# Kernel optimization log

Measured on AMD Instinct MI355X. Metric: run time of the kernel, lower is better.

The kernel has to match this reference:

```python
import jax, jax.numpy as jnp
import numpy as np

# ---- MERU-style Lorentz geometry helpers (space components, implicit time) ----

def _time(x, curv):
    # x: [..., D] space component; time = sqrt(1/curv + ||x||^2)
    return jnp.sqrt(1.0 / curv + jnp.sum(x * x, axis=-1))


def pairwise_dist(x, y, curv, eps=1e-8):
    # Lorentzian inner product for all pairs: <x,y>_L = x.y - x_t*y_t  -> [N, M]
    xt = _time(x, curv)
    yt = _time(y, curv)
    inner = jnp.einsum('nd,md->nm', x, y) - xt[:, None] * yt[None, :]
    c_xyl = -curv * inner  # >= 1 on the hyperboloid
    return jnp.arccosh(jnp.clip(c_xyl, 1.0 + eps, None)) / jnp.sqrt(curv)


def oxy_angle(x, y, curv, eps=1e-8):
    # exterior angle at x of geodesic triangle (origin, x, y); elementwise over batch
    xt = _time(x, curv)
    yt = _time(y, curv)
    c_xyl = curv * (jnp.sum(x * y, axis=-1) - xt * yt)  # <= -1
    acos_numer = yt + c_xyl * xt
    acos_denom = jnp.linalg.norm(x, axis=-1) * jnp.sqrt(jnp.clip(c_xyl * c_xyl - 1.0, 0.0, None))
    acos_input = acos_numer / (acos_denom + eps)
    return jnp.arccos(jnp.clip(acos_input, -1.0 + eps, 1.0 - eps))


def half_aperture(x, curv, min_radius=0.1, eps=1e-6):
    asin_input = 2.0 * min_radius / (jnp.linalg.norm(x, axis=-1) * jnp.sqrt(curv) + eps)
    return jnp.arcsin(jnp.clip(asin_input, -1.0 + eps, 1.0 - eps))


def soft_cross_entropy(logits, target_probs):
    # torch.nn.CrossEntropyLoss with probability targets (rows need not sum to 1)
    return jnp.mean(-jnp.sum(target_probs * jax.nn.log_softmax(logits, axis=-1), axis=-1))


def entailment_loss(fa, fb, curv, eps=1e-6):
    ang = oxy_angle(fa, fb, curv)
    ap = half_aperture(fa, curv, eps=eps)
    return jnp.mean(jnp.clip(ang - ap, 0.0, None))


def setup_inputs() -> dict:
    key = jax.random.key(0)
    k1, k2, k3, k4 = jax.random.split(key, 4)
    B, D = 4096, 512
    return {
        'image_features': jax.random.normal(k1, (B, D), dtype=jnp.float32),
        'dna_features': jax.random.normal(k2, (B, D), dtype=jnp.float32),
        'text_features': jax.random.normal(k3, (B, D), dtype=jnp.float32),
        'labels': jax.random.randint(k4, (B,), 0, 500, dtype=jnp.int64),
        'logit_scale': jnp.float32(10.0),
        'curv': jnp.float32(1.0),
    }


ENTAIL_WEIGHT = 0.2


def reference(image_features, dna_features, text_features, labels, logit_scale, curv):
    # world_size == 1: gathered features == local features
    label_mat = (labels[None, :] == labels[:, None]).astype(jnp.float32)  # [B, B]

    feats = [image_features, dna_features, text_features]  # idx 0=image, 1=dna, 2=text

    contrastive_losses = []
    entail_losses = []
    for ia in range(3):
        for ib in range(3):
            if ia == ib:
                continue
            sim_ab = -pairwise_dist(feats[ia], feats[ib], curv)
            sim_ba = -pairwise_dist(feats[ib], feats[ia], curv)
            contrastive_losses.append(soft_cross_entropy(logit_scale * sim_ab, label_mat))
            contrastive_losses.append(soft_cross_entropy(logit_scale * sim_ba, label_mat))
            # 2D features branch: entailment only for (dna, image) ordering
            if ia == 1 and ib == 0:
                entail_losses.append(entailment_loss(feats[1], feats[0], curv, eps=1e-6))
            elif ia == 0 and ib == 1:
                entail_losses.append(entailment_loss(feats[1], feats[0], curv, eps=1e-6))

    contrastive_total = sum(contrastive_losses) / len(contrastive_losses)
    entail_total = sum(entail_losses) / len(entail_losses)
    total = contrastive_total + ENTAIL_WEIGHT * entail_total
    return total, contrastive_total, entail_total
```

## Files before the change

### kernel.cpp

```cpp
#include <hip/hip_runtime.h>
#include <stdint.h>

#define B_SZ 4096
#define D_SZ 512
#define SHIFT 64.0f

typedef __attribute__((ext_vector_type(4))) float floatx4;
typedef __attribute__((ext_vector_type(2))) long lng2;
typedef unsigned char u8;
typedef unsigned int u32;

#define GLD_LDS16(gp, sp)                                                              \
    __builtin_amdgcn_global_load_lds(                                                  \
        (const __attribute__((address_space(1))) void*)(gp),                           \
        (__attribute__((address_space(3))) void*)(sp), 16, 0, 0)

#define FP8MFMA(accv, av, bv)                                                          \
    accv = __builtin_amdgcn_mfma_f32_16x16x32_fp8_fp8(av, bv, accv, 0, 0, 0)

__global__ __launch_bounds__(256) void prep_kernel(
    const float* __restrict__ img, const float* __restrict__ dna,
    const float* __restrict__ txt, const float* __restrict__ curv_p,
    const int* __restrict__ labels, int* __restrict__ hist,
    u8* __restrict__ f8, float* __restrict__ times,
    float* __restrict__ zero_f, float* __restrict__ ent_partial) {
    __shared__ int lhist[512];
    __shared__ float red[4];
    int t = threadIdx.x;
    int gid = blockIdx.x * 256 + t;
    if (gid < 49155) zero_f[gid] = 0.0f;

    if (blockIdx.x == 0) {
        lhist[t] = 0; lhist[t + 256] = 0;
        __syncthreads();
        for (int n = t; n < B_SZ; n += 256) atomicAdd(&lhist[labels[n]], 1);
        __syncthreads();
        hist[t] = lhist[t]; hist[t + 256] = lhist[t + 256];
    }

    int wave = gid >> 6;
    int lane = t & 63;
    const float* src = (wave < B_SZ) ? img : (wave < 2 * B_SZ) ? dna : txt;
    int row = wave & (B_SZ - 1);
    const float* p = src + row * D_SZ + lane * 8;
    float4 v0 = *(const float4*)(p);
    float4 v1 = *(const float4*)(p + 4);
    float ss = v0.x*v0.x + v0.y*v0.y + v0.z*v0.z + v0.w*v0.w
             + v1.x*v1.x + v1.y*v1.y + v1.z*v1.z + v1.w*v1.w;
    u32 w0 = __builtin_amdgcn_cvt_pk_fp8_f32(v0.x, v0.y, 0, false);
    w0 = __builtin_amdgcn_cvt_pk_fp8_f32(v0.z, v0.w, w0, true);
    u32 w1 = __builtin_amdgcn_cvt_pk_fp8_f32(v1.x, v1.y, 0, false);
    w1 = __builtin_amdgcn_cvt_pk_fp8_f32(v1.z, v1.w, w1, true);
    uint2 pk; pk.x = w0; pk.y = w1;
    int gperm = (lane & 56) | ((lane & 3) << 1) | ((lane >> 2) & 1);
    *(uint2*)(f8 + (size_t)wave * D_SZ + gperm * 8) = pk;

    bool isdna = (wave >= B_SZ) && (wave < 2 * B_SZ);
    float dot = 0.0f, ssy = 0.0f;
    if (isdna) {
        const float* y = img + row * D_SZ + lane * 8;
        float4 y0 = *(const float4*)y, y1 = *(const float4*)(y + 4);
        dot = v0.x*y0.x + v0.y*y0.y + v0.z*y0.z + v0.w*y0.w
            + v1.x*y1.x + v1.y*y1.y + v1.z*y1.z + v1.w*y1.w;
        ssy = y0.x*y0.x + y0.y*y0.y + y0.z*y0.z + y0.w*y0.w
            + y1.x*y1.x + y1.y*y1.y + y1.z*y1.z + y1.w*y1.w;
    }
    #pragma unroll
    for (int m = 1; m < 64; m <<= 1) {
        ss += __shfl_xor(ss, m);
        if (isdna) { dot += __shfl_xor(dot, m); ssy += __shfl_xor(ssy, m); }
    }
    float curv = curv_p[0];
    float ep = 0.0f;
    if (lane == 0) {
        float xt = sqrtf(1.0f / curv + ss);
        times[wave] = xt;
        if (isdna) {
            float yt = sqrtf(1.0f / curv + ssy);
            float nx = sqrtf(ss);
            float c = curv * (dot - xt * yt);
            float numer = yt + c * xt;
            float denom = nx * sqrtf(fmaxf(c * c - 1.0f, 0.0f));
            float ai = numer / (denom + 1e-8f);
            ai = fminf(fmaxf(ai, -1.0f + 1e-8f), 1.0f - 1e-8f);
            float ang = acosf(ai);
            float as_in = 0.2f / (nx * sqrtf(curv) + 1e-6f);
            as_in = fminf(fmaxf(as_in, -1.0f + 1e-6f), 1.0f - 1e-6f);
            float ap = asinf(as_in);
            ep = fmaxf(ang - ap, 0.0f);
        }
    }
    if (blockIdx.x >= 1024 && blockIdx.x < 2048) {
        if (lane == 0) red[t >> 6] = ep;
        __syncthreads();
        if (t == 0) ent_partial[blockIdx.x - 1024] = red[0] + red[1] + red[2] + red[3];
    }
}

__global__ __launch_bounds__(512, 4) void gemm_epi_kernel(
    const u8* __restrict__ f8, const float* __restrict__ times,
    const int* __restrict__ labels,
    const float* __restrict__ ls_p, const float* __restrict__ curv_p,
    float* __restrict__ rsum_e, float* __restrict__ rsum_t,
    float* __restrict__ csum_e, float* __restrict__ csum_t) {
    __shared__ u8 sA[3][256 * 64];
    __shared__ u8 sB[3][128 * 64];

    int z = blockIdx.z;
    int pa = (z == 2) ? 1 : 0;
    int pb = (z == 0) ? 1 : 2;
    const u8* A  = f8 + (size_t)pa * (B_SZ * D_SZ);
    const u8* Bm = f8 + (size_t)pb * (B_SZ * D_SZ);

    int t = threadIdx.x;
    int rowBlk = blockIdx.y * 256;
    int colBlk = blockIdx.x * 128;
    int wave = t >> 6, lane = t & 63;
    int rq  = wave >> 1;
    int chh = wave & 1;

    int lrow = lane >> 2;
    int lch  = (lane & 3) ^ ((lane >> 3) & 3);
    const u8* gA0 = A  + (size_t)(rowBlk + wave * 32 + lrow)      * D_SZ + lch * 16;
    const u8* gA1 = A  + (size_t)(rowBlk + wave * 32 + 16 + lrow) * D_SZ + lch * 16;
    const u8* gB  = Bm + (size_t)(colBlk + wave * 16 + lrow)      * D_SZ + lch * 16;

    int q = lane >> 4, s = lane & 15;
    int slot16 = (q ^ ((s >> 1) & 3)) << 4;
    int aBase = (rq * 64 + s) * 64 + slot16;
    int bBase = (chh * 64 + s) * 64 + slot16;

    floatx4 acc[4][4];
    #pragma unroll
    for (int ii = 0; ii < 4; ++ii)
        #pragma unroll
        for (int j = 0; j < 4; ++j) acc[ii][j] = (floatx4){0.f, 0.f, 0.f, 0.f};

    {
        GLD_LDS16(gA0,      &sA[0][wave * 2048]);
        GLD_LDS16(gA1,      &sA[0][wave * 2048 + 1024]);
        GLD_LDS16(gB,       &sB[0][wave * 1024]);
        GLD_LDS16(gA0 + 64, &sA[1][wave * 2048]);
        GLD_LDS16(gA1 + 64, &sA[1][wave * 2048 + 1024]);
        GLD_LDS16(gB  + 64, &sB[1][wave * 1024]);
    }

    #pragma unroll
    for (int si = 0; si < D_SZ / 64; ++si) {
        const int cur = si % 3;
        const u8* pA = &sA[cur][0];
        const u8* pB = &sB[cur][0];
        if (si < 7) { asm volatile("s_waitcnt vmcnt(3)" ::: "memory"); }
        else        { asm volatile("s_waitcnt vmcnt(0)" ::: "memory"); }
        asm volatile("s_barrier" ::: "memory");

        lng2 a0 = *(const lng2*)(pA + aBase);
        lng2 a1 = *(const lng2*)(pA + aBase + 1024);
        lng2 a2 = *(const lng2*)(pA + aBase + 2048);
        lng2 a3 = *(const lng2*)(pA + aBase + 3072);
        lng2 b0 = *(const lng2*)(pB + bBase);
        lng2 b1 = *(const lng2*)(pB + bBase + 1024);
        if (si < 6) {
            const int nb = (si + 2) % 3;
            const int ko = (si + 2) * 64;
            GLD_LDS16(gA0 + ko, &sA[nb][wave * 2048]);
            GLD_LDS16(gA1 + ko, &sA[nb][wave * 2048 + 1024]);
        }
        asm volatile("s_barrier" ::: "memory");
        asm volatile("s_waitcnt lgkmcnt(0)" ::: "memory");
        __builtin_amdgcn_s_setprio(1);
        FP8MFMA(acc[0][0], a0.x, b0.x); FP8MFMA(acc[0][1], a0.x, b1.x);
        FP8MFMA(acc[1][0], a1.x, b0.x); FP8MFMA(acc[1][1], a1.x, b1.x);
        FP8MFMA(acc[2][0], a2.x, b0.x); FP8MFMA(acc[2][1], a2.x, b1.x);
        FP8MFMA(acc[3][0], a3.x, b0.x); FP8MFMA(acc[3][1], a3.x, b1.x);
        FP8MFMA(acc[0][0], a0.y, b0.y); FP8MFMA(acc[0][1], a0.y, b1.y);
        FP8MFMA(acc[1][0], a1.y, b0.y); FP8MFMA(acc[1][1], a1.y, b1.y);
        FP8MFMA(acc[2][0], a2.y, b0.y); FP8MFMA(acc[2][1], a2.y, b1.y);
        FP8MFMA(acc[3][0], a3.y, b0.y); FP8MFMA(acc[3][1], a3.y, b1.y);
        __builtin_amdgcn_s_setprio(0);
        asm volatile("s_barrier" ::: "memory");

        lng2 b2 = *(const lng2*)(pB + bBase + 2048);
        lng2 b3 = *(const lng2*)(pB + bBase + 3072);
        if (si < 6) {
            const int nb = (si + 2) % 3;
            const int ko = (si + 2) * 64;
            GLD_LDS16(gB + ko, &sB[nb][wave * 1024]);
        }
        asm volatile("s_barrier" ::: "memory");
        asm volatile("s_waitcnt lgkmcnt(0)" ::: "memory");
        __builtin_amdgcn_s_setprio(1);
        FP8MFMA(acc[0][2], a0.x, b2.x); FP8MFMA(acc[0][3], a0.x, b3.x);
        FP8MFMA(acc[1][2], a1.x, b2.x); FP8MFMA(acc[1][3], a1.x, b3.x);
        FP8MFMA(acc[2][2], a2.x, b2.x); FP8MFMA(acc[2][3], a2.x, b3.x);
        FP8MFMA(acc[3][2], a3.x, b2.x); FP8MFMA(acc[3][3], a3.x, b3.x);
        FP8MFMA(acc[0][2], a0.y, b2.y); FP8MFMA(acc[0][3], a0.y, b3.y);
        FP8MFMA(acc[1][2], a1.y, b2.y); FP8MFMA(acc[1][3], a1.y, b3.y);
        FP8MFMA(acc[2][2], a2.y, b2.y); FP8MFMA(acc[2][3], a2.y, b3.y);
        FP8MFMA(acc[3][2], a3.y, b2.y); FP8MFMA(acc[3][3], a3.y, b3.y);
        __builtin_amdgcn_s_setprio(0);
    }

    float ls = ls_p[0];
    float curv = curv_p[0];
    float rsc = rsqrtf(curv);
    float c2 = -ls * rsc;
    float c1 = c2 * 0.69314718f;
    float sh2p = SHIFT * 1.44269504f + c2;
    const float* tA = times + pa * B_SZ;
    const float* tB = times + pb * B_SZ;

    int rowbase = rowBlk + rq * 64;
    int colbase = colBlk + chh * 64;

    float tb[4]; int lb[4]; int mcol[4];
    #pragma unroll
    for (int j = 0; j < 4; ++j) {
        mcol[j] = colbase + j * 16 + s;
        tb[j] = tB[mcol[j]];
        lb[j] = labels[mcol[j]];
    }
    float colE[4] = {0.f, 0.f, 0.f, 0.f}, colT[4] = {0.f, 0.f, 0.f, 0.f};

    float* rsE = rsum_e + z * B_SZ;
    float* rsT = rsum_t + z * B_SZ;
    float* csE = csum_e + z * B_SZ;
    float* csT = csum_t + z * B_SZ;

    #pragma unroll
    for (int ii = 0; ii < 4; ++ii) {
        int nb = rowbase + ii * 16 + q * 4;
        float cta[4]; int la[4];
        #pragma unroll
        for (int r = 0; r < 4; ++r) { cta[r] = curv * tA[nb + r]; la[r] = labels[nb + r]; }
        float re[4] = {0.f, 0.f, 0.f, 0.f}, rt[4] = {0.f, 0.f, 0.f, 0.f};
        #pragma unroll
        for (int j = 0; j < 4; ++j) {
            floatx4 a = acc[ii][j];
            #pragma unroll
            for (int r = 0; r < 4; ++r) {
                float zc = fmaf(-curv, a[r], cta[r] * tb[j]);
                zc = fmaxf(zc, 1.0f + 1e-8f);
                float lz = __log2f(zc);
                float e = __builtin_amdgcn_exp2f(fmaf(c2, lz, sh2p));
                float tl = (la[r] == lb[j]) ? fmaf(c1, lz, c1) : 0.0f;
                re[r] += e; rt[r] += tl;
                colE[j] += e; colT[j] += tl;
            }
        }
        #pragma unroll
        for (int r = 0; r < 4; ++r) {
            #pragma unroll
            for (int m = 1; m <= 8; m <<= 1) {
                re[r] += __shfl_xor(re[r], m);
                rt[r] += __shfl_xor(rt[r], m);
            }
        }
        #pragma unroll
        for (int r = 0; r < 4; ++r) {
            if (s == r) {
                atomicAdd(&rsE[nb + r], re[r]);
                atomicAdd(&rsT[nb + r], rt[r]);
            }
        }
    }
    #pragma unroll
    for (int j = 0; j < 4; ++j) {
        colE[j] += __shfl_xor(colE[j], 16); colE[j] += __shfl_xor(colE[j], 32);
        colT[j] += __shfl_xor(colT[j], 16); colT[j] += __shfl_xor(colT[j], 32);
        if (q == 0) {
            atomicAdd(&csE[mcol[j]], colE[j]);
            atomicAdd(&csT[mcol[j]], colT[j]);
        }
    }
}

__global__ __launch_bounds__(256) void finalize_kernel(
    const float* __restrict__ rsum_e, const float* __restrict__ rsum_t,
    const float* __restrict__ csum_e, const float* __restrict__ csum_t,
    const int* __restrict__ labels, const int* __restrict__ hist,
    const float* __restrict__ ent_partial,
    float* __restrict__ ce_acc, float* __restrict__ ent_acc,
    int* __restrict__ done, float* __restrict__ out) {
    __shared__ float red[4], red2[4];
    int b = blockIdx.x, tid = threadIdx.x;
    int n = b * 256 + tid;
    float Sn = (float)hist[labels[n]];
    float part = 0.0f;
    #pragma unroll
    for (int p = 0; p < 3; ++p) {
        part += Sn * (__logf(rsum_e[p * B_SZ + n]) - SHIFT) - rsum_t[p * B_SZ + n];
        part += Sn * (__logf(csum_e[p * B_SZ + n]) - SHIFT) - csum_t[p * B_SZ + n];
    }
    float ep = (b < 4) ? ent_partial[b * 256 + tid] : 0.0f;
    #pragma unroll
    for (int m = 1; m < 64; m <<= 1) {
        part += __shfl_xor(part, m);
        ep   += __shfl_xor(ep, m);
    }
    if ((tid & 63) == 0) { red[tid >> 6] = part; red2[tid >> 6] = ep; }
    __syncthreads();
    if (tid == 0) {
        atomicAdd(ce_acc, red[0] + red[1] + red[2] + red[3]);
        atomicAdd(ent_acc, red2[0] + red2[1] + red2[2] + red2[3]);
        __threadfence();
        if (atomicAdd(done, 1) == 15) {
            float ce = atomicAdd(ce_acc, 0.0f);
            float ent = atomicAdd(ent_acc, 0.0f);
            float contr = ce / (6.0f * (float)B_SZ);
            ent /= (float)B_SZ;
            out[0] = contr + 0.2f * ent;
            out[1] = contr;
            out[2] = ent;
        }
    }
}

extern "C" void kernel_launch(void* const* d_in, const int* in_sizes, int n_in,
                              void* d_out, int out_size, void* d_ws, size_t ws_size,
                              hipStream_t stream) {
    const float* img    = (const float*)d_in[0];
    const float* dna    = (const float*)d_in[1];
    const float* txt    = (const float*)d_in[2];
    const int*   labels = (const int*)d_in[3];
    const float* ls     = (const float*)d_in[4];
    const float* curv   = (const float*)d_in[5];

    char* ws = (char*)d_ws;
    u8*    f8     = (u8*)ws;
    float* times  = (float*)(ws + 6291456);
    float* rsum_e = (float*)(ws + 6340608);
    float* rsum_t = (float*)(ws + 6389760);
    float* csum_e = (float*)(ws + 6438912);
    float* csum_t = (float*)(ws + 6488064);
    float* ce_acc = (float*)(ws + 6537216);
    float* ent_acc= (float*)(ws + 6537220);
    int*   done   = (int*)  (ws + 6537224);
    float* ent_p  = (float*)(ws + 6537228);
    int*   hist   = (int*)  (ws + 6541324);

    prep_kernel<<<3072, 256, 0, stream>>>(img, dna, txt, curv, labels, hist,
                                          f8, times, rsum_e, ent_p);
    dim3 g(32, 16, 3);
    gemm_epi_kernel<<<g, 512, 0, stream>>>(f8, times, labels, ls, curv,
                                           rsum_e, rsum_t, csum_e, csum_t);
    finalize_kernel<<<16, 256, 0, stream>>>(rsum_e, rsum_t, csum_e, csum_t,
                                            labels, hist, ent_p,
                                            ce_acc, ent_acc, done, (float*)d_out);
}
```

Measured before the change: 170.8 us.

## Enlarge GEMM tile to 256x256 with swizzled block order and four-phase pipeline

Doubles the column tile of the FP8 GEMM block from 128 to 256, so each wave computes 128x64 outputs (8x4 MFMA accumulators) and the grid halves. Block indices are remapped so consecutive blocks share operand rows, improving L2 reuse. The K-step is split into four MFMA clusters, each overlapped with one async global-to-LDS load, and the explicit lgkmcnt waits are dropped. This cuts LDS and global traffic per FLOP but raises register pressure and LDS use (occupancy hint removed) and leaves only 768 blocks.

```diff
diff --git a/kernel.cpp b/kernel.cpp
--- a/kernel.cpp
+++ b/kernel.cpp
@@ -97,14 +97,14 @@
     }
 }
 
-__global__ __launch_bounds__(512, 4) void gemm_epi_kernel(
+__global__ __launch_bounds__(512) void gemm_epi_kernel(
     const u8* __restrict__ f8, const float* __restrict__ times,
     const int* __restrict__ labels,
     const float* __restrict__ ls_p, const float* __restrict__ curv_p,
     float* __restrict__ rsum_e, float* __restrict__ rsum_t,
     float* __restrict__ csum_e, float* __restrict__ csum_t) {
     __shared__ u8 sA[3][256 * 64];
-    __shared__ u8 sB[3][128 * 64];
+    __shared__ u8 sB[3][256 * 64];
 
     int z = blockIdx.z;
     int pa = (z == 2) ? 1 : 0;
@@ -112,92 +112,100 @@
     const u8* A  = f8 + (size_t)pa * (B_SZ * D_SZ);
     const u8* Bm = f8 + (size_t)pb * (B_SZ * D_SZ);
 
+    int l  = blockIdx.y * 16 + blockIdx.x;
+    int tl = (l & 7) * 32 + (l >> 3);
+    int rowBlk = (tl >> 4) * 256;
+    int colBlk = (tl & 15) * 256;
+
     int t = threadIdx.x;
-    int rowBlk = blockIdx.y * 256;
-    int colBlk = blockIdx.x * 128;
     int wave = t >> 6, lane = t & 63;
-    int rq  = wave >> 1;
-    int chh = wave & 1;
+    int wr = wave >> 2;
+    int wc = wave & 3;
 
     int lrow = lane >> 2;
     int lch  = (lane & 3) ^ ((lane >> 3) & 3);
-    const u8* gA0 = A  + (size_t)(rowBlk + wave * 32 + lrow)      * D_SZ + lch * 16;
-    const u8* gA1 = A  + (size_t)(rowBlk + wave * 32 + 16 + lrow) * D_SZ + lch * 16;
-    const u8* gB  = Bm + (size_t)(colBlk + wave * 16 + lrow)      * D_SZ + lch * 16;
+    const u8* gA0 = A  + (size_t)(rowBlk + wave * 32 + lrow) * D_SZ + lch * 16;
+    const u8* gA1 = gA0 + 16 * D_SZ;
+    const u8* gB0 = Bm + (size_t)(colBlk + wave * 32 + lrow) * D_SZ + lch * 16;
+    const u8* gB1 = gB0 + 16 * D_SZ;
 
     int q = lane >> 4, s = lane & 15;
     int slot16 = (q ^ ((s >> 1) & 3)) << 4;
-    int aBase = (rq * 64 + s) * 64 + slot16;
-    int bBase = (chh * 64 + s) * 64 + slot16;
-
-    floatx4 acc[4][4];
-    #pragma unroll
-    for (int ii = 0; ii < 4; ++ii)
+    int aBase = (wr * 128 + s) * 64 + slot16;
+    int bBase = (wc * 64  + s) * 64 + slot16;
+
+    floatx4 acc[8][4];
+    #pragma unroll
+    for (int ii = 0; ii < 8; ++ii)
         #pragma unroll
         for (int j = 0; j < 4; ++j) acc[ii][j] = (floatx4){0.f, 0.f, 0.f, 0.f};
 
     {
         GLD_LDS16(gA0,      &sA[0][wave * 2048]);
         GLD_LDS16(gA1,      &sA[0][wave * 2048 + 1024]);
-        GLD_LDS16(gB,       &sB[0][wave * 1024]);
+        GLD_LDS16(gB0,      &sB[0][wave * 2048]);
+        GLD_LDS16(gB1,      &sB[0][wave * 2048 + 1024]);
         GLD_LDS16(gA0 + 64, &sA[1][wave * 2048]);
         GLD_LDS16(gA1 + 64, &sA[1][wave * 2048 + 1024]);
-        GLD_LDS16(gB  + 64, &sB[1][wave * 1024]);
-    }
+        GLD_LDS16(gB0 + 64, &sB[1][wave * 2048]);
+        GLD_LDS16(gB1 + 64, &sB[1][wave * 2048 + 1024]);
+    }
+
+#define CLUSTER16(r0, r1, ae, ao)                                                      \
+    FP8MFMA(acc[r0][0], ae.x, b0.x); FP8MFMA(acc[r0][1], ae.x, b1.x);                  \
+    FP8MFMA(acc[r0][2], ae.x, b2.x); FP8MFMA(acc[r0][3], ae.x, b3.x);                  \
+    FP8MFMA(acc[r1][0], ao.x, b0.x); FP8MFMA(acc[r1][1], ao.x, b1.x);                  \
+    FP8MFMA(acc[r1][2], ao.x, b2.x); FP8MFMA(acc[r1][3], ao.x, b3.x);                  \
+    FP8MFMA(acc[r0][0], ae.y, b0.y); FP8MFMA(acc[r0][1], ae.y, b1.y);                  \
+    FP8MFMA(acc[r0][2], ae.y, b2.y); FP8MFMA(acc[r0][3], ae.y, b3.y);                  \
+    FP8MFMA(acc[r1][0], ao.y, b0.y); FP8MFMA(acc[r1][1], ao.y, b1.y);                  \
+    FP8MFMA(acc[r1][2], ao.y, b2.y); FP8MFMA(acc[r1][3], ao.y, b3.y);
 
     #pragma unroll
     for (int si = 0; si < D_SZ / 64; ++si) {
         const int cur = si % 3;
+        const int nxb = (si + 2) % 3;
+        const int ko  = (si + 2) * 64;
         const u8* pA = &sA[cur][0];
         const u8* pB = &sB[cur][0];
-        if (si < 7) { asm volatile("s_waitcnt vmcnt(3)" ::: "memory"); }
+        if (si < 7) { asm volatile("s_waitcnt vmcnt(4)" ::: "memory"); }
         else        { asm volatile("s_waitcnt vmcnt(0)" ::: "memory"); }
         asm volatile("s_barrier" ::: "memory");
 
         lng2 a0 = *(const lng2*)(pA + aBase);
         lng2 a1 = *(const lng2*)(pA + aBase + 1024);
+        lng2 b0 = *(const lng2*)(pB + bBase);
+        lng2 b1 = *(const lng2*)(pB + bBase + 1024);
+        lng2 b2 = *(const lng2*)(pB + bBase + 2048);
+        lng2 b3 = *(const lng2*)(pB + bBase + 3072);
+        if (si < 6) GLD_LDS16(gA0 + ko, &sA[nxb][wave * 2048]);
+        asm volatile("s_barrier" ::: "memory");
+        __builtin_amdgcn_s_setprio(1);
+        CLUSTER16(0, 1, a0, a1);
+        __builtin_amdgcn_s_setprio(0);
+
         lng2 a2 = *(const lng2*)(pA + aBase + 2048);
         lng2 a3 = *(const lng2*)(pA + aBase + 3072);
-        lng2 b0 = *(const lng2*)(pB + bBase);
-        lng2 b1 = *(const lng2*)(pB + bBase + 1024);
-        if (si < 6) {
-            const int nb = (si + 2) % 3;
-            const int ko = (si + 2) * 64;
-            GLD_LDS16(gA0 + ko, &sA[nb][wave * 2048]);
-            GLD_LDS16(gA1 + ko, &sA[nb][wave * 2048 + 1024]);
-        }
-        asm volatile("s_barrier" ::: "memory");
-        asm volatile("s_waitcnt lgkmcnt(0)" ::: "memory");
+        if (si < 6) GLD_LDS16(gA1 + ko, &sA[nxb][wave * 2048 + 1024]);
+        asm volatile("s_barrier" ::: "memory");
         __builtin_amdgcn_s_setprio(1);
-        FP8MFMA(acc[0][0], a0.x, b0.x); FP8MFMA(acc[0][1], a0.x, b1.x);
-        FP8MFMA(acc[1][0], a1.x, b0.x); FP8MFMA(acc[1][1], a1.x, b1.x);
-        FP8MFMA(acc[2][0], a2.x, b0.x); FP8MFMA(acc[2][1], a2.x, b1.x);
-        FP8MFMA(acc[3][0], a3.x, b0.x); FP8MFMA(acc[3][1], a3.x, b1.x);
-        FP8MFMA(acc[0][0], a0.y, b0.y); FP8MFMA(acc[0][1], a0.y, b1.y);
-        FP8MFMA(acc[1][0], a1.y, b0.y); FP8MFMA(acc[1][1], a1.y, b1.y);
-        FP8MFMA(acc[2][0], a2.y, b0.y); FP8MFMA(acc[2][1], a2.y, b1.y);
-        FP8MFMA(acc[3][0], a3.y, b0.y); FP8MFMA(acc[3][1], a3.y, b1.y);
+        CLUSTER16(2, 3, a2, a3);
         __builtin_amdgcn_s_setprio(0);
-        asm volatile("s_barrier" ::: "memory");
-
-        lng2 b2 = *(const lng2*)(pB + bBase + 2048);
-        lng2 b3 = *(const lng2*)(pB + bBase + 3072);
-        if (si < 6) {
-            const int nb = (si + 2) % 3;
-            const int ko = (si + 2) * 64;
-            GLD_LDS16(gB + ko, &sB[nb][wave * 1024]);
-        }
-        asm volatile("s_barrier" ::: "memory");
-        asm volatile("s_waitcnt lgkmcnt(0)" ::: "memory");
+
+        lng2 a4 = *(const lng2*)(pA + aBase + 4096);
+        lng2 a5 = *(const lng2*)(pA + aBase + 5120);
+        if (si < 6) GLD_LDS16(gB0 + ko, &sB[nxb][wave * 2048]);
+        asm volatile("s_barrier" ::: "memory");
         __builtin_amdgcn_s_setprio(1);
-        FP8MFMA(acc[0][2], a0.x, b2.x); FP8MFMA(acc[0][3], a0.x, b3.x);
-        FP8MFMA(acc[1][2], a1.x, b2.x); FP8MFMA(acc[1][3], a1.x, b3.x);
-        FP8MFMA(acc[2][2], a2.x, b2.x); FP8MFMA(acc[2][3], a2.x, b3.x);
-        FP8MFMA(acc[3][2], a3.x, b2.x); FP8MFMA(acc[3][3], a3.x, b3.x);
-        FP8MFMA(acc[0][2], a0.y, b2.y); FP8MFMA(acc[0][3], a0.y, b3.y);
-        FP8MFMA(acc[1][2], a1.y, b2.y); FP8MFMA(acc[1][3], a1.y, b3.y);
-        FP8MFMA(acc[2][2], a2.y, b2.y); FP8MFMA(acc[2][3], a2.y, b3.y);
-        FP8MFMA(acc[3][2], a3.y, b2.y); FP8MFMA(acc[3][3], a3.y, b3.y);
+        CLUSTER16(4, 5, a4, a5);
+        __builtin_amdgcn_s_setprio(0);
+
+        lng2 a6 = *(const lng2*)(pA + aBase + 6144);
+        lng2 a7 = *(const lng2*)(pA + aBase + 7168);
+        if (si < 6) GLD_LDS16(gB1 + ko, &sB[nxb][wave * 2048 + 1024]);
+        asm volatile("s_barrier" ::: "memory");
+        __builtin_amdgcn_s_setprio(1);
+        CLUSTER16(6, 7, a6, a7);
         __builtin_amdgcn_s_setprio(0);
     }
 
@@ -210,8 +218,8 @@
     const float* tA = times + pa * B_SZ;
     const float* tB = times + pb * B_SZ;
 
-    int rowbase = rowBlk + rq * 64;
-    int colbase = colBlk + chh * 64;
+    int rowbase = rowBlk + wr * 128;
+    int colbase = colBlk + wc * 64;
 
     float tb[4]; int lb[4]; int mcol[4];
     #pragma unroll
@@ -228,7 +236,7 @@
     float* csT = csum_t + z * B_SZ;
 
     #pragma unroll
-    for (int ii = 0; ii < 4; ++ii) {
+    for (int ii = 0; ii < 8; ++ii) {
         int nb = rowbase + ii * 16 + q * 4;
         float cta[4]; int la[4];
         #pragma unroll
@@ -243,9 +251,9 @@
                 zc = fmaxf(zc, 1.0f + 1e-8f);
                 float lz = __log2f(zc);
                 float e = __builtin_amdgcn_exp2f(fmaf(c2, lz, sh2p));
-                float tl = (la[r] == lb[j]) ? fmaf(c1, lz, c1) : 0.0f;
-                re[r] += e; rt[r] += tl;
-                colE[j] += e; colT[j] += tl;
+                float tl2 = (la[r] == lb[j]) ? fmaf(c1, lz, c1) : 0.0f;
+                re[r] += e; rt[r] += tl2;
+                colE[j] += e; colT[j] += tl2;
             }
         }
         #pragma unroll
@@ -341,7 +349,7 @@
 
     prep_kernel<<<3072, 256, 0, stream>>>(img, dna, txt, curv, labels, hist,
                                           f8, times, rsum_e, ent_p);
-    dim3 g(32, 16, 3);
+    dim3 g(16, 16, 3);
     gemm_epi_kernel<<<g, 512, 0, stream>>>(f8, times, labels, ls, curv,
                                            rsum_e, rsum_t, csum_e, csum_t);
     finalize_kernel<<<16, 256, 0, stream>>>(rsum_e, rsum_t, csum_e, csum_t,
```

Measured after the change: 200.1 us. 17.2% more time.
